# Performance work log

Measured on AMD Instinct MI355X. Metric: run time of the kernel, lower is better.

Reference implementation:

```python
import jax, jax.numpy as jnp
import numpy as np
from jax import lax

B = 32
NUM_CLASSES = 80
NUM_ANCHORS = 3
IMG_SIZE = 320
STRIDES = (8, 16, 32)
TOPK = 1000
CONF_THRESH = 0.05
NMS_THRESH = 0.6
EPS = 1e-10

ANCHOR_SIZES = np.array([[16, 16], [32, 32], [64, 48],
                         [64, 64], [96, 96], [128, 96],
                         [128, 128], [192, 160], [256, 256]],
                        dtype=np.float32).reshape(3, NUM_ANCHORS, 2)


def _build_anchors():
    # mirrors YOWOv3.generate_anchors
    boxes, strides = [], []
    for lvl, s in enumerate(STRIDES):
        f = IMG_SIZE // s
        ys, xs = np.meshgrid(np.arange(f), np.arange(f), indexing='ij')
        xy = np.stack([xs, ys], axis=-1).astype(np.float32).reshape(-1, 1, 2)
        xy = np.repeat(xy, NUM_ANCHORS, axis=1) * s            # [f*f, A, 2]
        wh = np.broadcast_to(ANCHOR_SIZES[lvl], (f * f, NUM_ANCHORS, 2))
        boxes.append(np.concatenate([xy, wh], axis=-1).reshape(-1, 4))
        strides.append(np.full(f * f * NUM_ANCHORS, s, dtype=np.float32))
    return np.concatenate(boxes, 0), np.concatenate(strides, 0)


def setup_inputs() -> dict:
    key = jax.random.key(0)
    k1, k2, k3 = jax.random.split(key, 3)
    anchors_np, stride_np = _build_anchors()
    M = anchors_np.shape[0]  # 6300
    conf_pred = jax.random.normal(k1, (B, M, 1), dtype=jnp.float32)
    cls_pred = jax.random.normal(k2, (B, M, NUM_CLASSES), dtype=jnp.float32) * 2.0
    reg_pred = jax.random.normal(k3, (B, M, 4), dtype=jnp.float32) * 0.5
    return {
        'conf_pred': conf_pred,
        'cls_pred': cls_pred,
        'reg_pred': reg_pred,
        'anchors': jnp.asarray(anchors_np),
        'stride_map': jnp.asarray(stride_np),
    }


def _decode_boxes(anchors, stride_map, reg_pred):
    # anchors [M,4] (cx, cy, w, h) in pixels; reg_pred [B,M,4]
    ctr = anchors[None, :, :2] + jax.nn.sigmoid(reg_pred[..., :2]) * stride_map[None, :, None]
    wh = anchors[None, :, 2:] * jnp.exp(reg_pred[..., 2:])
    return jnp.concatenate([ctr - 0.5 * wh, ctr + 0.5 * wh], axis=-1)  # [B,M,4] x1y1x2y2


def _nms_keep(boxes, scores, labels):
    # boxes [K,4] sorted by descending score; per-class greedy NMS -> bool keep [K]
    x1, y1, x2, y2 = boxes[:, 0], boxes[:, 1], boxes[:, 2], boxes[:, 3]
    areas = (x2 - x1) * (y2 - y1)
    xx1 = jnp.maximum(x1[:, None], x1[None, :])
    yy1 = jnp.maximum(y1[:, None], y1[None, :])
    xx2 = jnp.minimum(x2[:, None], x2[None, :])
    yy2 = jnp.minimum(y2[:, None], y2[None, :])
    inter = jnp.maximum(EPS, xx2 - xx1) * jnp.maximum(EPS, yy2 - yy1)
    union = jnp.maximum(areas[:, None] + areas[None, :] - inter, EPS)
    iou = inter / union
    suppress = (iou > NMS_THRESH) & (labels[:, None] == labels[None, :])
    keep0 = scores >= CONF_THRESH
    idxs = jnp.arange(boxes.shape[0])

    def body(i, keep):
        # if box i is kept, suppress all later same-class boxes with iou > thresh
        return keep & ~(keep[i] & suppress[i] & (idxs > i))

    return lax.fori_loop(0, boxes.shape[0], body, keep0)


def reference(conf_pred, cls_pred, reg_pred, anchors, stride_map):
    box_pred = _decode_boxes(anchors, stride_map, reg_pred)              # [B,M,4]
    joint = jax.nn.sigmoid(conf_pred) * jax.nn.softmax(cls_pred, -1)     # [B,M,C]
    scores = jnp.max(joint, axis=-1)                                     # [B,M]
    labels = jnp.argmax(joint, axis=-1)                                  # [B,M]

    top_scores, top_idx = lax.top_k(scores, TOPK)                        # sorted desc
    top_labels = jnp.take_along_axis(labels, top_idx, axis=1)
    top_boxes = jnp.take_along_axis(box_pred, top_idx[..., None], axis=1)
    top_boxes = jnp.clip(top_boxes / IMG_SIZE, 0.0, 1.0)                 # [B,K,4]

    keep = jax.vmap(_nms_keep)(top_boxes, top_scores, top_labels)        # [B,K] bool
    return top_scores, top_labels, top_boxes, keep
```

## Files before the change

### kernel.cpp

```cpp
#include <hip/hip_runtime.h>
#include <stdint.h>

#define NB 32
#define NM 6300
#define NC 80
#define NTOP 1000
#define NPAD 1024
#define NCAND 2048
#define NBINS 4096

static constexpr float IMGSZ   = 320.0f;
static constexpr float CONF_TH = 0.05f;
static constexpr float NMS_TH  = 0.6f;
static constexpr float EPSF    = 1e-10f;

static constexpr size_t OFF_SCORES = 0;
static constexpr size_t OFF_LABELS = OFF_SCORES + (size_t)NB * NM * 4;
static constexpr size_t OFF_TIDX   = OFF_LABELS + (size_t)NB * NM * 4;
static constexpr size_t OFF_NBOX   = OFF_TIDX   + (size_t)NB * NPAD * 4;
static constexpr size_t OFF_NLAB   = OFF_NBOX   + (size_t)NB * NPAD * 16;
static constexpr size_t OFF_SUP    = ((OFF_NLAB + (size_t)NB * NPAD * 4) + 1023) & ~(size_t)1023;

__global__ __launch_bounds__(256) void k_score(const float* __restrict__ conf,
                                               const float* __restrict__ cls,
                                               float* __restrict__ scores,
                                               int* __restrict__ labels) {
#pragma clang fp contract(off)
    int t = blockIdx.x * blockDim.x + threadIdx.x;
    int a = t >> 4;
    int l = t & 15;
    if (a >= NB * NM) return;
    const float* row = cls + (size_t)a * NC;

    float v[5];
#pragma unroll
    for (int k = 0; k < 5; ++k) v[k] = row[l + 16 * k];

    float bv = v[0];
    int bi = l;
#pragma unroll
    for (int k = 1; k < 5; ++k) {
        int c = l + 16 * k;
        if (v[k] > bv) { bv = v[k]; bi = c; }
    }
#pragma unroll
    for (int m = 1; m < 16; m <<= 1) {
        float ov = __shfl_xor(bv, m, 16);
        int   oi = __shfl_xor(bi, m, 16);
        if (ov > bv || (ov == bv && oi < bi)) { bv = ov; bi = oi; }
    }
    float s = 0.0f;
#pragma unroll
    for (int k = 0; k < 5; ++k) s += expf(v[k] - bv);
#pragma unroll
    for (int m = 1; m < 16; m <<= 1) s += __shfl_xor(s, m, 16);

    if (l == 0) {
        float cf  = conf[a];
        float sig = 1.0f / (1.0f + expf(-cf));
        float inv = 1.0f / s;
        scores[a] = sig * inv;
        labels[a] = bi;
    }
}

__global__ __launch_bounds__(1024) void k_topk(const float* __restrict__ scores,
                                               float* __restrict__ out_scores,
                                               int* __restrict__ top_idx) {
    __shared__ uint32_t hist[NBINS];
    __shared__ __align__(16) uint64_t key[NCAND];
    __shared__ int sT, scnt;
    int b = blockIdx.x, tid = threadIdx.x;
    const float* sb = scores + (size_t)b * NM;

    for (int i = tid; i < NBINS; i += 1024) hist[i] = 0;
    for (int i = tid; i < NCAND; i += 1024) key[i] = 0;
    if (tid == 0) scnt = 0;
    __syncthreads();

    for (int i = tid; i < NM; i += 1024)
        atomicAdd(&hist[__float_as_uint(sb[i]) >> 20], 1u);
    __syncthreads();

    if (tid < 64) {
        int l = tid;
        uint32_t q = 0;
        for (int i = 0; i < 64; ++i) q += hist[l * 64 + i];
        uint32_t s = q;
        for (int off = 1; off < 64; off <<= 1) {
            uint32_t o = __shfl_down(s, off);
            if (l + off < 64) s += o;
        }
        uint64_t m = __ballot(s >= (uint32_t)NTOP);
        int c = 63 - __clzll(m);
        uint32_t sc_ = __shfl(s, c);
        uint32_t qc  = __shfl(q, c);
        uint32_t tail = sc_ - qc;
        uint32_t v = hist[c * 64 + l];
        uint32_t s2 = v;
        for (int off = 1; off < 64; off <<= 1) {
            uint32_t o = __shfl_down(s2, off);
            if (l + off < 64) s2 += o;
        }
        uint64_t m2 = __ballot(s2 + tail >= (uint32_t)NTOP);
        int T = c * 64 + (63 - __clzll(m2));
        if (l == 0) sT = T;
    }
    __syncthreads();

    uint32_t T = (uint32_t)sT;
    int lane = tid & 63;
    for (int i = tid; i < NM; i += 1024) {
        uint32_t bits = __float_as_uint(sb[i]);
        bool pred = (bits >> 20) >= T;
        uint64_t mask = __ballot(pred);
        if (pred) {
            int leader = __ffsll((unsigned long long)mask) - 1;
            int prefix = __popcll(mask & ((1ull << lane) - 1));
            int base = 0;
            if (lane == leader) base = atomicAdd(&scnt, (int)__popcll(mask));
            base = __shfl(base, leader);
            int pos = base + prefix;
            if (pos < NCAND)
                key[pos] = ((uint64_t)bits << 32) | (uint32_t)(~(uint32_t)i);
        }
    }
    __syncthreads();

    int C = scnt; if (C > NCAND) C = NCAND;
    int C2 = (C + 1) >> 1;
    const ulonglong2* k2 = (const ulonglong2*)key;
    for (int t = tid; t < C; t += 1024) {
        uint64_t kt = key[t];
        uint32_t rank = 0;
        for (int j = 0; j < C2; ++j) {
            ulonglong2 kk = k2[j];
            rank += (kk.x > kt) ? 1u : 0u;
            rank += (kk.y > kt) ? 1u : 0u;
        }
        if (rank < (uint32_t)NTOP) {
            out_scores[b * NTOP + rank] = __uint_as_float((uint32_t)(kt >> 32));
            top_idx[b * NPAD + rank]    = (int)(~(uint32_t)kt);
        }
    }
}

__global__ __launch_bounds__(256) void k_decode(const int* __restrict__ top_idx,
                                                const int* __restrict__ labels,
                                                const float* __restrict__ reg,
                                                const float* __restrict__ anchors,
                                                const float* __restrict__ stridemap,
                                                float* __restrict__ out_labels,
                                                float* __restrict__ out_boxes,
                                                float* __restrict__ nbox,
                                                int* __restrict__ nlab) {
#pragma clang fp contract(off)
    int t = blockIdx.x * blockDim.x + threadIdx.x;
    if (t >= NB * NTOP) return;
    int b = t / NTOP, r = t % NTOP;
    int idx = top_idx[b * NPAD + r];
    int lab = labels[(size_t)b * NM + idx];
    out_labels[b * NTOP + r] = (float)lab;

    const float* rg = reg + ((size_t)b * NM + idx) * 4;
    float rx = rg[0], ry = rg[1], rw = rg[2], rh = rg[3];
    const float* an = anchors + (size_t)idx * 4;
    float ax = an[0], ay = an[1], aw = an[2], ah = an[3];
    float st = stridemap[idx];

    float sx = 1.0f / (1.0f + expf(-rx));
    float sy = 1.0f / (1.0f + expf(-ry));
    float cx = ax + sx * st;
    float cy = ay + sy * st;
    float w  = aw * expf(rw);
    float h  = ah * expf(rh);
    float x1 = cx - 0.5f * w, y1 = cy - 0.5f * h;
    float x2 = cx + 0.5f * w, y2 = cy + 0.5f * h;

    float nx1 = fminf(fmaxf(x1 / IMGSZ, 0.0f), 1.0f);
    float ny1 = fminf(fmaxf(y1 / IMGSZ, 0.0f), 1.0f);
    float nx2 = fminf(fmaxf(x2 / IMGSZ, 0.0f), 1.0f);
    float ny2 = fminf(fmaxf(y2 / IMGSZ, 0.0f), 1.0f);

    float4 bx = make_float4(nx1, ny1, nx2, ny2);
    ((float4*)out_boxes)[b * NTOP + r] = bx;
    ((float4*)nbox)[b * NPAD + r]      = bx;
    nlab[b * NPAD + r] = lab;
}

__global__ __launch_bounds__(256) void k_supmat(const float* __restrict__ nbox,
                                                const int* __restrict__ nlab,
                                                uint64_t* __restrict__ sup) {
#pragma clang fp contract(off)
    int b = blockIdx.y;
    int t = blockIdx.x;
    int tj = (int)((sqrtf(8.0f * (float)t + 1.0f) - 1.0f) * 0.5f);
    while ((tj + 1) * (tj + 2) / 2 <= t) ++tj;
    while (tj * (tj + 1) / 2 > t) --tj;
    int ti = t - tj * (tj + 1) / 2;

    int lane = threadIdx.x & 63;
    int w    = threadIdx.x >> 6;

    int i = ti * 64 + lane;
    int j = tj * 64 + lane;

    float4 bi = ((const float4*)nbox)[b * NPAD + i];
    float  ai = (bi.z - bi.x) * (bi.w - bi.y);
    int    li = nlab[b * NPAD + i];
    float4 bj = ((const float4*)nbox)[b * NPAD + j];
    int    lj = nlab[b * NPAD + j];
    bool   iv = (i < NTOP);

    uint64_t mybits = 0;
#pragma unroll
    for (int u = 0; u < 16; ++u) {
        int jj = (w << 4) | u;
        float bjx = __shfl(bj.x, jj);
        float bjy = __shfl(bj.y, jj);
        float bjz = __shfl(bj.z, jj);
        float bjw = __shfl(bj.w, jj);
        int   ljv = __shfl(lj, jj);
        float ajv = (bjz - bjx) * (bjw - bjy);
        int   jg  = tj * 64 + jj;
        float xx1 = fmaxf(bi.x, bjx);
        float yy1 = fmaxf(bi.y, bjy);
        float xx2 = fminf(bi.z, bjz);
        float yy2 = fminf(bi.w, bjw);
        float inter = fmaxf(EPSF, xx2 - xx1) * fmaxf(EPSF, yy2 - yy1);
        float uni   = fmaxf(ai + ajv - inter, EPSF);
        float iou   = inter / uni;
        bool pred = (i < jg) && iv && (jg < NTOP) && (li == ljv) && (iou > NMS_TH);
        uint64_t bal = __ballot(pred);
        if (lane == jj) mybits = bal;
    }
    if ((lane >> 4) == w)
        sup[(((size_t)b * 16 + tj) * 16 + ti) * 64 + lane] = mybits;
}

__global__ __launch_bounds__(1024) void k_nms(const float* __restrict__ out_scores,
                                              const uint64_t* __restrict__ sup,
                                              float* __restrict__ out_keep) {
    __shared__ uint64_t Kw[16];
    int b    = blockIdx.x;
    int w    = threadIdx.x >> 6;
    int lane = threadIdx.x & 63;
    const uint64_t* supb = sup + (size_t)b * 16 * 16 * 64;

    uint64_t wrow[16];
#pragma unroll
    for (int ti = 0; ti < 16; ++ti)
        wrow[ti] = (ti <= w) ? supb[((size_t)w * 16 + ti) * 64 + lane] : 0ULL;

    int pos = w * 64 + lane;
    bool k0 = (pos < NTOP) && (out_scores[b * NTOP + pos] >= CONF_TH);

    uint64_t ext = 0;
#pragma unroll
    for (int s = 0; s < 16; ++s) {
        if (w == s) {
            bool cand = k0 && (ext == 0ULL);
            uint64_t wself = wrow[s];
            uint64_t alive = __ballot(cand);
            for (int it = 0; it < 64; ++it) {
                bool dead = (wself & alive) != 0ULL;
                uint64_t na = __ballot(cand && !dead);
                if (na == alive) break;
                alive = na;
            }
            if (lane == 0) Kw[s] = alive;
            if (pos < NTOP)
                out_keep[b * NTOP + pos] = ((alive >> lane) & 1ULL) ? 1.0f : 0.0f;
        }
        __syncthreads();
        if (w > s) ext |= wrow[s] & Kw[s];
    }
}

extern "C" void kernel_launch(void* const* d_in, const int* in_sizes, int n_in,
                              void* d_out, int out_size, void* d_ws, size_t ws_size,
                              hipStream_t stream) {
    const float* conf = (const float*)d_in[0];
    const float* cls  = (const float*)d_in[1];
    const float* reg  = (const float*)d_in[2];
    const float* anch = (const float*)d_in[3];
    const float* strm = (const float*)d_in[4];

    float* out        = (float*)d_out;
    float* out_scores = out;
    float* out_labels = out + NB * NTOP;
    float* out_boxes  = out + 2 * NB * NTOP;
    float* out_keep   = out + 2 * NB * NTOP + NB * NTOP * 4;

    char* ws = (char*)d_ws;
    float*    scores = (float*)(ws + OFF_SCORES);
    int*      labels = (int*)(ws + OFF_LABELS);
    int*      tidx   = (int*)(ws + OFF_TIDX);
    float*    nbox   = (float*)(ws + OFF_NBOX);
    int*      nlab   = (int*)(ws + OFF_NLAB);
    uint64_t* sup    = (uint64_t*)(ws + OFF_SUP);

    k_score<<<(NB * NM * 16) / 256, 256, 0, stream>>>(conf, cls, scores, labels);
    k_topk<<<NB, 1024, 0, stream>>>(scores, out_scores, tidx);
    k_decode<<<(NB * NTOP + 255) / 256, 256, 0, stream>>>(tidx, labels, reg, anch, strm,
                                                          out_labels, out_boxes, nbox, nlab);
    k_supmat<<<dim3(136, NB), 256, 0, stream>>>(nbox, nlab, sup);
    k_nms<<<NB, 1024, 0, stream>>>(out_scores, sup, out_keep);
}
```

Before: 80.33 us.

## Fuse box decode into top-k kernel and register-block the rank counting

Removes the separate decode kernel by having the top-k kernel decode and write boxes, labels and NMS inputs directly at each candidate's rank. This drops one launch and the top_idx round-trip through global memory. The rank loop now has each thread hold two candidate keys and compare them against 16 shared keys per step, so every LDS read serves two ranks. The histogram prefix sum staggers its reads per lane to avoid LDS bank conflicts. In exchange the decode runs on only 32 blocks, which limits parallelism for the gather and exp work.

```diff
diff --git a/kernel.cpp b/kernel.cpp
--- a/kernel.cpp
+++ b/kernel.cpp
@@ -16,8 +16,7 @@
 
 static constexpr size_t OFF_SCORES = 0;
 static constexpr size_t OFF_LABELS = OFF_SCORES + (size_t)NB * NM * 4;
-static constexpr size_t OFF_TIDX   = OFF_LABELS + (size_t)NB * NM * 4;
-static constexpr size_t OFF_NBOX   = OFF_TIDX   + (size_t)NB * NPAD * 4;
+static constexpr size_t OFF_NBOX   = OFF_LABELS + (size_t)NB * NM * 4;
 static constexpr size_t OFF_NLAB   = OFF_NBOX   + (size_t)NB * NPAD * 16;
 static constexpr size_t OFF_SUP    = ((OFF_NLAB + (size_t)NB * NPAD * 4) + 1023) & ~(size_t)1023;
 
@@ -65,8 +64,16 @@
 }
 
 __global__ __launch_bounds__(1024) void k_topk(const float* __restrict__ scores,
+                                               const int* __restrict__ labels,
+                                               const float* __restrict__ reg,
+                                               const float* __restrict__ anchors,
+                                               const float* __restrict__ stridemap,
                                                float* __restrict__ out_scores,
-                                               int* __restrict__ top_idx) {
+                                               float* __restrict__ out_labels,
+                                               float* __restrict__ out_boxes,
+                                               float* __restrict__ nbox,
+                                               int* __restrict__ nlab) {
+#pragma clang fp contract(off)
     __shared__ uint32_t hist[NBINS];
     __shared__ __align__(16) uint64_t key[NCAND];
     __shared__ int sT, scnt;
@@ -74,7 +81,7 @@
     const float* sb = scores + (size_t)b * NM;
 
     for (int i = tid; i < NBINS; i += 1024) hist[i] = 0;
-    for (int i = tid; i < NCAND; i += 1024) key[i] = 0;
+    key[tid] = 0; key[tid + 1024] = 0;
     if (tid == 0) scnt = 0;
     __syncthreads();
 
@@ -85,7 +92,7 @@
     if (tid < 64) {
         int l = tid;
         uint32_t q = 0;
-        for (int i = 0; i < 64; ++i) q += hist[l * 64 + i];
+        for (int k = 0; k < 64; ++k) q += hist[l * 64 + ((k + l) & 63)];
         uint32_t s = q;
         for (int off = 1; off < 64; off <<= 1) {
             uint32_t o = __shfl_down(s, off);
@@ -128,64 +135,60 @@
     __syncthreads();
 
     int C = scnt; if (C > NCAND) C = NCAND;
-    int C2 = (C + 1) >> 1;
-    const ulonglong2* k2 = (const ulonglong2*)key;
-    for (int t = tid; t < C; t += 1024) {
-        uint64_t kt = key[t];
-        uint32_t rank = 0;
-        for (int j = 0; j < C2; ++j) {
-            ulonglong2 kk = k2[j];
-            rank += (kk.x > kt) ? 1u : 0u;
-            rank += (kk.y > kt) ? 1u : 0u;
-        }
-        if (rank < (uint32_t)NTOP) {
-            out_scores[b * NTOP + rank] = __uint_as_float((uint32_t)(kt >> 32));
-            top_idx[b * NPAD + rank]    = (int)(~(uint32_t)kt);
-        }
-    }
-}
-
-__global__ __launch_bounds__(256) void k_decode(const int* __restrict__ top_idx,
-                                                const int* __restrict__ labels,
-                                                const float* __restrict__ reg,
-                                                const float* __restrict__ anchors,
-                                                const float* __restrict__ stridemap,
-                                                float* __restrict__ out_labels,
-                                                float* __restrict__ out_boxes,
-                                                float* __restrict__ nbox,
-                                                int* __restrict__ nlab) {
-#pragma clang fp contract(off)
-    int t = blockIdx.x * blockDim.x + threadIdx.x;
-    if (t >= NB * NTOP) return;
-    int b = t / NTOP, r = t % NTOP;
-    int idx = top_idx[b * NPAD + r];
-    int lab = labels[(size_t)b * NM + idx];
-    out_labels[b * NTOP + r] = (float)lab;
-
-    const float* rg = reg + ((size_t)b * NM + idx) * 4;
-    float rx = rg[0], ry = rg[1], rw = rg[2], rh = rg[3];
-    const float* an = anchors + (size_t)idx * 4;
-    float ax = an[0], ay = an[1], aw = an[2], ah = an[3];
-    float st = stridemap[idx];
-
-    float sx = 1.0f / (1.0f + expf(-rx));
-    float sy = 1.0f / (1.0f + expf(-ry));
-    float cx = ax + sx * st;
-    float cy = ay + sy * st;
-    float w  = aw * expf(rw);
-    float h  = ah * expf(rh);
-    float x1 = cx - 0.5f * w, y1 = cy - 0.5f * h;
-    float x2 = cx + 0.5f * w, y2 = cy + 0.5f * h;
-
-    float nx1 = fminf(fmaxf(x1 / IMGSZ, 0.0f), 1.0f);
-    float ny1 = fminf(fmaxf(y1 / IMGSZ, 0.0f), 1.0f);
-    float nx2 = fminf(fmaxf(x2 / IMGSZ, 0.0f), 1.0f);
-    float ny2 = fminf(fmaxf(y2 / IMGSZ, 0.0f), 1.0f);
-
-    float4 bx = make_float4(nx1, ny1, nx2, ny2);
-    ((float4*)out_boxes)[b * NTOP + r] = bx;
-    ((float4*)nbox)[b * NPAD + r]      = bx;
-    nlab[b * NPAD + r] = lab;
+    int Cr = (C + 15) & ~15;
+    uint64_t kt0 = key[tid];
+    uint64_t kt1 = key[tid + 1024];
+    uint32_t r0 = 0, r1 = 0;
+    for (int j = 0; j < Cr; j += 16) {
+        const ulonglong2* k2 = (const ulonglong2*)(key + j);
+        ulonglong2 a0 = k2[0], a1 = k2[1], a2 = k2[2], a3 = k2[3];
+        ulonglong2 a4 = k2[4], a5 = k2[5], a6 = k2[6], a7 = k2[7];
+        r0 += (a0.x > kt0) + (a0.y > kt0) + (a1.x > kt0) + (a1.y > kt0);
+        r0 += (a2.x > kt0) + (a2.y > kt0) + (a3.x > kt0) + (a3.y > kt0);
+        r0 += (a4.x > kt0) + (a4.y > kt0) + (a5.x > kt0) + (a5.y > kt0);
+        r0 += (a6.x > kt0) + (a6.y > kt0) + (a7.x > kt0) + (a7.y > kt0);
+        r1 += (a0.x > kt1) + (a0.y > kt1) + (a1.x > kt1) + (a1.y > kt1);
+        r1 += (a2.x > kt1) + (a2.y > kt1) + (a3.x > kt1) + (a3.y > kt1);
+        r1 += (a4.x > kt1) + (a4.y > kt1) + (a5.x > kt1) + (a5.y > kt1);
+        r1 += (a6.x > kt1) + (a6.y > kt1) + (a7.x > kt1) + (a7.y > kt1);
+    }
+
+#pragma unroll
+    for (int cpick = 0; cpick < 2; ++cpick) {
+        uint64_t kt   = cpick ? kt1 : kt0;
+        uint32_t rank = cpick ? r1  : r0;
+        if (rank >= (uint32_t)NTOP) continue;
+        uint32_t sbits = (uint32_t)(kt >> 32);
+        int idx = (int)(~(uint32_t)kt);
+        out_scores[b * NTOP + rank] = __uint_as_float(sbits);
+        int lab = labels[(size_t)b * NM + idx];
+        out_labels[b * NTOP + rank] = (float)lab;
+
+        const float* rg = reg + ((size_t)b * NM + idx) * 4;
+        float rx = rg[0], ry = rg[1], rw = rg[2], rh = rg[3];
+        const float* an = anchors + (size_t)idx * 4;
+        float ax = an[0], ay = an[1], aw = an[2], ah = an[3];
+        float st = stridemap[idx];
+
+        float sx = 1.0f / (1.0f + expf(-rx));
+        float sy = 1.0f / (1.0f + expf(-ry));
+        float cx = ax + sx * st;
+        float cy = ay + sy * st;
+        float w  = aw * expf(rw);
+        float h  = ah * expf(rh);
+        float x1 = cx - 0.5f * w, y1 = cy - 0.5f * h;
+        float x2 = cx + 0.5f * w, y2 = cy + 0.5f * h;
+
+        float nx1 = fminf(fmaxf(x1 / IMGSZ, 0.0f), 1.0f);
+        float ny1 = fminf(fmaxf(y1 / IMGSZ, 0.0f), 1.0f);
+        float nx2 = fminf(fmaxf(x2 / IMGSZ, 0.0f), 1.0f);
+        float ny2 = fminf(fmaxf(y2 / IMGSZ, 0.0f), 1.0f);
+
+        float4 bx = make_float4(nx1, ny1, nx2, ny2);
+        ((float4*)out_boxes)[b * NTOP + rank] = bx;
+        ((float4*)nbox)[b * NPAD + rank]      = bx;
+        nlab[b * NPAD + rank] = lab;
+    }
 }
 
 __global__ __launch_bounds__(256) void k_supmat(const float* __restrict__ nbox,
@@ -295,15 +298,13 @@
     char* ws = (char*)d_ws;
     float*    scores = (float*)(ws + OFF_SCORES);
     int*      labels = (int*)(ws + OFF_LABELS);
-    int*      tidx   = (int*)(ws + OFF_TIDX);
     float*    nbox   = (float*)(ws + OFF_NBOX);
     int*      nlab   = (int*)(ws + OFF_NLAB);
     uint64_t* sup    = (uint64_t*)(ws + OFF_SUP);
 
     k_score<<<(NB * NM * 16) / 256, 256, 0, stream>>>(conf, cls, scores, labels);
-    k_topk<<<NB, 1024, 0, stream>>>(scores, out_scores, tidx);
-    k_decode<<<(NB * NTOP + 255) / 256, 256, 0, stream>>>(tidx, labels, reg, anch, strm,
-                                                          out_labels, out_boxes, nbox, nlab);
+    k_topk<<<NB, 1024, 0, stream>>>(scores, labels, reg, anch, strm,
+                                    out_scores, out_labels, out_boxes, nbox, nlab);
     k_supmat<<<dim3(136, NB), 256, 0, stream>>>(nbox, nlab, sup);
     k_nms<<<NB, 1024, 0, stream>>>(out_scores, sup, out_keep);
 }
```

Result: slower. 89.25 us (+11.1%).
